# Performance work log

Hardware: AMD Instinct MI355X
Metric: run time of the kernel (lower is better)

## Reference

```python
import jax, jax.numpy as jnp
import numpy as np

D_MODEL, D_INNER, D_STATE, NHEADS, HEADDIM, D_CONV, CHUNK = 1024, 2048, 128, 32, 64, 4, 64
B_SZ, L = 2, 2048
EPS = 1e-5


def _segsum_exp(x):
    # x: (..., T) -> exp of lower-triangular cumulative segment sums, (..., T, T)
    cs = jnp.cumsum(x, axis=-1)
    seg = cs[..., :, None] - cs[..., None, :]
    T = x.shape[-1]
    mask = jnp.tril(jnp.ones((T, T), dtype=bool))
    return jnp.exp(jnp.where(mask, seg, 0.0)) * mask


def ssd(x, A, B, C, chunk):
    # x: (b,l,h,p), A: (b,l,h), B,C: (b,l,n)
    b, l, h, p = x.shape
    n = B.shape[-1]
    c = l // chunk
    x = x.reshape(b, c, chunk, h, p)
    A = A.reshape(b, c, chunk, h).transpose(0, 3, 1, 2)        # (b,h,c,s)
    B = B.reshape(b, c, chunk, n)
    C = C.reshape(b, c, chunk, n)
    A_cum = jnp.cumsum(A, axis=-1)                              # (b,h,c,s)
    Lmat = _segsum_exp(A)                                       # (b,h,c,s,s)
    # intra-chunk (diagonal block) output
    Y_diag = jnp.einsum('bcln,bcsn,bhcls,bcshp->bclhp', C, B, Lmat, x)
    # per-chunk final states
    decay_states = jnp.exp(A_cum[..., -1:] - A_cum)             # (b,h,c,s)
    states = jnp.einsum('bcsn,bhcs,bcshp->bchpn', B, decay_states, x)
    states = jnp.concatenate([jnp.zeros_like(states[:, :1]), states], axis=1)  # (b,c+1,h,p,n)
    # inter-chunk recurrence over chunk sums
    chunk_sums = jnp.pad(A_cum[..., -1], ((0, 0), (0, 0), (1, 0)))  # (b,h,c+1)
    decay_chunk = _segsum_exp(chunk_sums)                       # (b,h,c+1,c+1)
    new_states = jnp.einsum('bhzc,bchpn->bzhpn', decay_chunk, states)
    states_in, final_state = new_states[:, :-1], new_states[:, -1]
    out_decay = jnp.exp(A_cum)                                  # (b,h,c,s)
    Y_off = jnp.einsum('bcln,bchpn,bhcl->bclhp', C, states_in, out_decay)
    Y = (Y_diag + Y_off).reshape(b, l, h, p)
    return Y, final_state


def causal_depthwise_conv(x, w, b):
    # x: (B, C, L), w: (C, K), b: (C,)
    K = w.shape[-1]
    Llen = x.shape[-1]
    xp = jnp.pad(x, ((0, 0), (0, 0), (K - 1, 0)))
    out = b[None, :, None]
    for k in range(K):
        out = out + w[None, :, k, None] * xp[:, :, k:k + Llen]
    return out


def setup_inputs() -> dict:
    key = jax.random.key(0)
    ks = jax.random.split(key, 9)
    d_in_proj = 2 * D_INNER + 2 * D_STATE + NHEADS
    conv_dim = D_INNER + 2 * D_STATE
    return {
        'u': jax.random.normal(ks[0], (B_SZ, L, D_MODEL), jnp.float32),
        'W_in': jax.random.normal(ks[1], (d_in_proj, D_MODEL), jnp.float32) * (D_MODEL ** -0.5),
        'conv_w': jax.random.normal(ks[2], (conv_dim, D_CONV), jnp.float32) * (D_CONV ** -0.5),
        'conv_b': jax.random.normal(ks[3], (conv_dim,), jnp.float32) * 0.01,
        'dt_bias': jax.random.normal(ks[4], (NHEADS,), jnp.float32),
        'A_log': jnp.log(1.0 + 15.0 * jax.random.uniform(ks[5], (NHEADS,), jnp.float32)),
        'D': jax.random.normal(ks[6], (NHEADS,), jnp.float32),
        'norm_w': jnp.ones((D_INNER,), jnp.float32),
        'W_out': jax.random.normal(ks[8], (D_MODEL, D_INNER), jnp.float32) * (D_INNER ** -0.5),
    }


def reference(u, W_in, conv_w, conv_b, dt_bias, A_log, D, norm_w, W_out):
    zxbcdt = u @ W_in.T                                        # (B,L,d_in_proj)
    z = zxbcdt[..., :D_INNER]
    xBC = zxbcdt[..., D_INNER:2 * D_INNER + 2 * D_STATE]
    dt = jax.nn.softplus(zxbcdt[..., -NHEADS:] + dt_bias)      # (B,L,H)
    # causal depthwise conv + silu
    xBC = causal_depthwise_conv(xBC.transpose(0, 2, 1), conv_w, conv_b).transpose(0, 2, 1)
    xBC = jax.nn.silu(xBC)
    A = -jnp.exp(A_log)                                        # (H,)
    x = xBC[..., :D_INNER].reshape(u.shape[0], u.shape[1], NHEADS, HEADDIM)
    Bm = xBC[..., D_INNER:D_INNER + D_STATE]
    Cm = xBC[..., D_INNER + D_STATE:]
    y, _ = ssd(x * dt[..., None], A * dt, Bm, Cm, CHUNK)
    y = y + x * D[:, None]
    y = y.reshape(u.shape[0], u.shape[1], D_INNER)
    # gated RMSNorm
    y = y * jax.nn.silu(z)
    y = y * jax.lax.rsqrt(jnp.mean(y * y, axis=-1, keepdims=True) + EPS) * norm_w
    return y @ W_out.T
```

## Files before the change

### kernel.cpp

```cpp
#include <hip/hip_runtime.h>
#include <hip/hip_bf16.h>
#include <math.h>

#define D_MODEL 1024
#define D_INNER 2048
#define D_STATE 128
#define NHEADS 32
#define HEADDIM 64
#define CHUNK 64
#define B_SZ 2
#define LSEQ 2048
#define BL (B_SZ*LSEQ)
#define DPROJ (2*D_INNER + 2*D_STATE + NHEADS)
#define CONV_DIM (D_INNER + 2*D_STATE)
#define NCHUNK (LSEQ/CHUNK)
#define NPAD1 4480
#define EPSF 1e-5f

typedef __attribute__((ext_vector_type(8))) _Float16 half8;
typedef __attribute__((ext_vector_type(4))) _Float16 half4;
typedef __attribute__((ext_vector_type(4))) float f32x4;

__device__ __forceinline__ float siluf(float v){ return v / (1.0f + expf(-v)); }
__device__ __forceinline__ float softplusf(float v){ return v > 20.0f ? v : log1pf(expf(v)); }
__device__ __forceinline__ unsigned short f2h(float x){
  union { _Float16 h; unsigned short u; } v; v.h = (_Float16)x;
  return v.u;
}
__device__ __forceinline__ float h2f(unsigned short x){
  union { unsigned short u; _Float16 h; } v; v.u = x;
  return (float)v.h;
}
__device__ __forceinline__ _Float16 h2h(unsigned short x){
  union { unsigned short u; _Float16 h; } v; v.u = x;
  return v.h;
}

typedef const __attribute__((address_space(1))) void gvoid_t;
typedef __attribute__((address_space(3))) void lvoid_t;
__device__ __forceinline__ void gl_lds16(const void* gsrc, void* ldst) {
  gvoid_t* g = reinterpret_cast<gvoid_t*>((uintptr_t)gsrc);
  lvoid_t* l = reinterpret_cast<lvoid_t*>((unsigned int)(uintptr_t)ldst);
  __builtin_amdgcn_global_load_lds(g, l, 16, 0, 0);
}

__global__ void cvt_f16(const float* __restrict__ in, unsigned short* __restrict__ out, int n4) {
  int i = blockIdx.x*256 + threadIdx.x;
  if (i >= n4) return;
  float4 v = *(const float4*)(in + (size_t)i*4);
  ushort4 o; o.x=f2h(v.x); o.y=f2h(v.y); o.z=f2h(v.z); o.w=f2h(v.w);
  *(ushort4*)(out + (size_t)i*4) = o;
}

__global__ void cvt_pad(const float* __restrict__ in, unsigned short* __restrict__ out,
                        int rows_in, int total4, int kdim4) {
  int i = blockIdx.x*256 + threadIdx.x;
  if (i >= total4) return;
  int row = i / kdim4;
  ushort4 o; o.x=0; o.y=0; o.z=0; o.w=0;
  if (row < rows_in) {
    float4 v = *(const float4*)(in + (size_t)i*4);
    o.x=f2h(v.x); o.y=f2h(v.y); o.z=f2h(v.z); o.w=f2h(v.w);
  }
  *(ushort4*)(out + (size_t)i*4) = o;
}

template<int OUT_F16>
__global__ __launch_bounds__(256) void gemm_f16_pipe(const unsigned short* __restrict__ A,
    const unsigned short* __restrict__ W, void* __restrict__ Cv, int N, int K) {
  __shared__ unsigned short lds[5*2*4096];
  const int t   = threadIdx.x;
  const int wid = t >> 6, l = t & 63;
  const int nwg = gridDim.x * gridDim.y;
  int bid = blockIdx.y * gridDim.x + blockIdx.x;
  int swz = (bid & 7) * (nwg >> 3) + (bid >> 3);
  const int m0 = (swz / gridDim.x) * 128;
  const int n0 = (swz % gridDim.x) * 128;
  const int wr = wid >> 1, wc = wid & 1;
  const int fr = l & 15, cg = l >> 4;
  const int NT = K >> 5;

  int srow[2]; int scol[2];
  #pragma unroll
  for (int i=0;i<2;++i){
    int s = i*256 + t;
    int r = s >> 2, c = s & 3;
    int sw = (r + (r>>2)) & 3;
    srow[i] = r; scol[i] = (c ^ sw) * 8;
  }
  const unsigned short* Abase = A + (size_t)m0 * K;
  const unsigned short* Wbase = W + (size_t)n0 * K;

#define STAGE(tt, slot) { \
    int kk = (tt) << 5; \
    unsigned short* La = &lds[(slot)*8192]; \
    unsigned short* Lb = &lds[(slot)*8192 + 4096]; \
    gl_lds16(Abase + (size_t)srow[0]*K + kk + scol[0], (char*)La + (0*256+t)*16); \
    gl_lds16(Abase + (size_t)srow[1]*K + kk + scol[1], (char*)La + (1*256+t)*16); \
    gl_lds16(Wbase + (size_t)srow[0]*K + kk + scol[0], (char*)Lb + (0*256+t)*16); \
    gl_lds16(Wbase + (size_t)srow[1]*K + kk + scol[1], (char*)Lb + (1*256+t)*16); \
  }

  f32x4 acc[4][4] = {};
  STAGE(0, 0);
  STAGE(1, 1);
  STAGE(2, 2);
  STAGE(3, 3);
  asm volatile("s_waitcnt vmcnt(12)" ::: "memory");
  __builtin_amdgcn_s_barrier();
  asm volatile("" ::: "memory");

  int cs = 0;
  for (int tt = 0; tt < NT; ++tt) {
    int ss = (cs == 0) ? 4 : cs - 1;
    if (tt + 4 < NT) STAGE(tt+4, ss);
    const unsigned short* La = &lds[cs*8192];
    const unsigned short* Lb = &lds[cs*8192 + 4096];
    half8 af[4], bfv[4];
    #pragma unroll
    for (int m=0;m<4;++m){
      int r = wr*64 + m*16 + fr;
      int sw = (r + (r>>2)) & 3;
      af[m] = *(const half8*)&La[(r*4 + (cg ^ sw))*8];
    }
    #pragma unroll
    for (int n=0;n<4;++n){
      int r = wc*64 + n*16 + fr;
      int sw = (r + (r>>2)) & 3;
      bfv[n] = *(const half8*)&Lb[(r*4 + (cg ^ sw))*8];
    }
    __builtin_amdgcn_s_setprio(1);
    #pragma unroll
    for (int m=0;m<4;++m)
      #pragma unroll
      for (int n=0;n<4;++n)
        acc[m][n] = __builtin_amdgcn_mfma_f32_16x16x32_f16(af[m], bfv[n], acc[m][n], 0, 0, 0);
    __builtin_amdgcn_s_setprio(0);
    if (tt + 1 < NT) {
      if      (tt + 4 < NT) { asm volatile("s_waitcnt vmcnt(12)" ::: "memory"); }
      else if (tt + 3 < NT) { asm volatile("s_waitcnt vmcnt(8)"  ::: "memory"); }
      else if (tt + 2 < NT) { asm volatile("s_waitcnt vmcnt(4)"  ::: "memory"); }
      else                  { asm volatile("s_waitcnt vmcnt(0)"  ::: "memory"); }
      __builtin_amdgcn_s_barrier();
      asm volatile("" ::: "memory");
    }
    cs = (cs == 4) ? 0 : cs + 1;
  }
#undef STAGE

  const int crow = m0 + wr*64 + (l >> 4) * 4;
  const int ccol0 = n0 + wc*64 + fr;
  #pragma unroll
  for (int m = 0; m < 4; ++m) {
    #pragma unroll
    for (int n = 0; n < 4; ++n) {
      int col = ccol0 + n*16;
      if (col < N) {
        if (OUT_F16) {
          unsigned short* cp = (unsigned short*)Cv + (size_t)(crow + m*16)*N + col;
          #pragma unroll
          for (int j = 0; j < 4; ++j) cp[(size_t)j*N] = f2h(acc[m][n][j]);
        } else {
          float* cp = (float*)Cv + (size_t)(crow + m*16)*N + col;
          #pragma unroll
          for (int j = 0; j < 4; ++j) cp[(size_t)j*N] = acc[m][n][j];
        }
      }
    }
  }
}

__global__ void dtx_kernel(const unsigned short* __restrict__ zx,
    const float* __restrict__ dt_bias, float* __restrict__ dt) {
  int i = blockIdx.x*256 + threadIdx.x;
  if (i >= BL*NHEADS) return;
  int row = i >> 5, h = i & 31;
  float v = h2f(zx[(size_t)row*DPROJ + (2*D_INNER + 2*D_STATE) + h]) + dt_bias[h];
  dt[i] = softplusf(v);
}

__global__ __launch_bounds__(64) void acum_kernel(const float* __restrict__ dt,
    const float* __restrict__ A_log, float* __restrict__ A_cum) {
  int blk = blockIdx.x;
  int c = blk & 31, h = (blk >> 5) & 31, b = blk >> 10;
  int l = threadIdx.x;
  __shared__ float sv[64];
  int row = b*LSEQ + c*CHUNK + l;
  float a = -expf(A_log[h]);
  sv[l] = a * dt[row*NHEADS + h];
  __syncthreads();
  if (l == 0) {
    float s = 0.f;
    for (int i=0;i<64;++i){ s += sv[i]; sv[i] = s; }
  }
  __syncthreads();
  A_cum[blk*64 + l] = sv[l];
}

__global__ __launch_bounds__(256) void conv8_kernel(const unsigned short* __restrict__ zx,
    const float* __restrict__ w, const float* __restrict__ bias, unsigned short* __restrict__ xBC) {
  int idx = blockIdx.x*256 + threadIdx.x;
  if (idx >= (BL/8)*(CONV_DIM/4)) return;
  int c4  = idx % (CONV_DIM/4);
  int rb  = idx / (CONV_DIM/4);
  int ch  = c4 * 4;
  int row0 = rb * 8;
  int l0   = row0 & (LSEQ-1);
  float4 r[11];
  #pragma unroll
  for (int jj=0;jj<11;++jj){
    int li = l0 + jj - 3;
    if (li >= 0) {
      ushort4 v = *(const ushort4*)&zx[(size_t)(row0 + jj - 3)*DPROJ + D_INNER + ch];
      r[jj] = make_float4(h2f(v.x), h2f(v.y), h2f(v.z), h2f(v.w));
    } else r[jj] = make_float4(0.f,0.f,0.f,0.f);
  }
  float4 wv[4];
  #pragma unroll
  for (int c=0;c<4;++c) wv[c] = *(const float4*)&w[(ch+c)*4];
  float4 bv = *(const float4*)&bias[ch];
  #pragma unroll
  for (int j=0;j<8;++j){
    float4 acc = bv;
    acc.x += wv[0].x*r[j].x + wv[0].y*r[j+1].x + wv[0].z*r[j+2].x + wv[0].w*r[j+3].x;
    acc.y += wv[1].x*r[j].y + wv[1].y*r[j+1].y + wv[1].z*r[j+2].y + wv[1].w*r[j+3].y;
    acc.z += wv[2].x*r[j].z + wv[2].y*r[j+1].z + wv[2].z*r[j+2].z + wv[2].w*r[j+3].z;
    acc.w += wv[3].x*r[j].w + wv[3].y*r[j+1].w + wv[3].z*r[j+2].w + wv[3].w*r[j+3].w;
    ushort4 o; o.x=f2h(siluf(acc.x)); o.y=f2h(siluf(acc.y)); o.z=f2h(siluf(acc.z)); o.w=f2h(siluf(acc.w));
    *(ushort4*)&xBC[(size_t)(row0+j)*CONV_DIM + ch] = o;
  }
}

__global__ __launch_bounds__(256) void g_kernel(const unsigned short* __restrict__ xBC, float* __restrict__ G) {
  int blk = blockIdx.x >> 2;
  int lq  = blockIdx.x & 3;
  int b = blk >> 5, c = blk & 31;
  __shared__ float Bsh[64][129];
  int t = threadIdx.x;
  int row0 = b*LSEQ + c*CHUNK;
  for (int j=0;j<32;++j){
    int lin = j*256 + t;
    int s = lin >> 7, n = lin & 127;
    Bsh[s][n] = h2f(xBC[(size_t)(row0+s)*CONV_DIM + D_INNER + n]);
  }
  __syncthreads();
  int l = lq*16 + (t >> 4), s0 = (t & 15) * 4;
  const unsigned short* Cp = &xBC[(size_t)(row0+l)*CONV_DIM + D_INNER + D_STATE];
  float acc[4] = {};
  for (int n=0;n<128;++n){
    float cv = h2f(Cp[n]);
    #pragma unroll
    for (int j=0;j<4;++j) acc[j] += cv * Bsh[s0+j][n];
  }
  float* Gp = &G[(size_t)blk*4096 + l*64 + s0];
  #pragma unroll
  for (int j=0;j<4;++j) Gp[j] = acc[j];
}

__global__ __launch_bounds__(256) void states_mfma(const unsigned short* __restrict__ xBC,
    const float* __restrict__ dt, const float* __restrict__ A_cum, unsigned short* __restrict__ states) {
  int blk = blockIdx.x;
  int h = blk & 31, c = (blk>>5)&31, b = blk>>10;
  __shared__ _Float16 Bt[128][72];
  __shared__ _Float16 xdT[64][72];
  __shared__ float Ac[64], dtl[64];
  int t = threadIdx.x;
  int wid = t >> 6, ln = t & 63;
  int row0 = b*LSEQ + c*CHUNK;
  if (t < 64){ Ac[t] = A_cum[((b*32+h)*32 + c)*64 + t]; dtl[t] = dt[(row0+t)*NHEADS + h]; }
  __syncthreads();
  float AcL = Ac[63];
  #pragma unroll
  for (int j=0;j<32;++j){
    int lin = j*256+t; int s = lin>>7, n = lin&127;
    Bt[n][s] = h2h(xBC[(size_t)(row0+s)*CONV_DIM + D_INNER + n]);
  }
  #pragma unroll
  for (int j=0;j<16;++j){
    int lin = j*256+t; int s = lin>>6, p = lin&63;
    xdT[p][s] = (_Float16)(h2f(xBC[(size_t)(row0+s)*CONV_DIM + h*HEADDIM + p]) * dtl[s] * expf(AcL - Ac[s]));
  }
  __syncthreads();
  const int fr = ln & 15, fk = (ln >> 4) * 8;
  f32x4 acc[4][2] = {};
  #pragma unroll
  for (int ks = 0; ks < 2; ++ks){
    half8 a[4], bb[2];
    #pragma unroll
    for (int pt=0;pt<4;++pt) a[pt] = *(const half8*)&xdT[pt*16+fr][ks*32+fk];
    #pragma unroll
    for (int nt=0;nt<2;++nt) bb[nt] = *(const half8*)&Bt[(wid*2+nt)*16+fr][ks*32+fk];
    #pragma unroll
    for (int pt=0;pt<4;++pt)
      #pragma unroll
      for (int nt=0;nt<2;++nt)
        acc[pt][nt] = __builtin_amdgcn_mfma_f32_16x16x32_f16(a[pt], bb[nt], acc[pt][nt], 0, 0, 0);
  }
  unsigned short* Sp = &states[(size_t)blk*8192];
  #pragma unroll
  for (int pt=0;pt<4;++pt){
    int p0 = pt*16 + (ln>>4)*4;
    #pragma unroll
    for (int nt=0;nt<2;++nt){
      int n = (wid*2+nt)*16 + fr;
      #pragma unroll
      for (int j=0;j<4;++j) Sp[(p0+j)*128 + n] = f2h(acc[pt][nt][j]);
    }
  }
}

__global__ __launch_bounds__(256) void scan_kernel(const float* __restrict__ A_cum,
                                                   unsigned short* __restrict__ states) {
  int g  = blockIdx.x & 7;
  int bh = blockIdx.x >> 3;
  int b = bh >> 5, h = bh & 31;
  int t = threadIdx.x;
  float S[4];
  #pragma unroll
  for (int j=0;j<4;++j) S[j] = 0.f;
  for (int c=0;c<NCHUNK;++c){
    float decay = expf(A_cum[((b*32+h)*32 + c)*64 + 63]);
    unsigned short* Sp = &states[(size_t)((b*32+c)*32 + h)*8192];
    #pragma unroll
    for (int j=0;j<4;++j){
      float tmp = h2f(Sp[(g*4+j)*256+t]);
      Sp[(g*4+j)*256+t] = f2h(S[j]);
      S[j] = S[j]*decay + tmp;
    }
  }
}

__global__ __launch_bounds__(256) void y_mfma(const unsigned short* __restrict__ xBC,
    const unsigned short* __restrict__ zx, const float* __restrict__ dt,
    const float* __restrict__ A_cum, const float* __restrict__ G,
    const unsigned short* __restrict__ states, const float* __restrict__ Dp,
    unsigned short* __restrict__ y_pre) {
  int blk = blockIdx.x;
  int h = blk & 31, c = (blk>>5)&31, b = blk>>10;
  __shared__ _Float16 Cl[64][136];
  __shared__ _Float16 Sin[64][136];
  __shared__ _Float16 Ms[64][72];
  __shared__ _Float16 xdT[64][72];
  __shared__ float Ac[64], dtl[64];
  int t = threadIdx.x;
  int wid = t >> 6, ln = t & 63;
  int row0 = b*LSEQ + c*CHUNK;
  if (t < 64){ Ac[t] = A_cum[((b*32+h)*32 + c)*64 + t]; dtl[t] = dt[(row0+t)*NHEADS + h]; }
  __syncthreads();
  #pragma unroll
  for (int j=0;j<32;++j){
    int lin = j*256+t; int l = lin>>7, n = lin&127;
    Cl[l][n] = (_Float16)(h2f(xBC[(size_t)(row0+l)*CONV_DIM + D_INNER + D_STATE + n]) * expf(Ac[l]));
  }
  {
    const unsigned short* Sg = &states[(size_t)blk*8192];
    #pragma unroll
    for (int j=0;j<8;++j){
      int elem = (j*256+t)*4; int p = elem>>7, n = elem&127;
      ushort4 v = *(const ushort4*)&Sg[elem];
      half4 hv = { h2h(v.x), h2h(v.y), h2h(v.z), h2h(v.w) };
      *(half4*)&Sin[p][n] = hv;
    }
  }
  #pragma unroll
  for (int j=0;j<16;++j){
    int lin = j*256+t; int s = lin>>6, p = lin&63;
    xdT[p][s] = (_Float16)(h2f(xBC[(size_t)(row0+s)*CONV_DIM + h*HEADDIM + p]) * dtl[s]);
  }
  {
    const float* Gp = &G[(size_t)(b*32+c)*4096];
    #pragma unroll
    for (int j=0;j<16;++j){
      int lin = j*256+t; int l = lin>>6, s = lin&63;
      Ms[l][s] = (s <= l) ? (_Float16)(Gp[l*64+s] * expf(Ac[l]-Ac[s])) : (_Float16)0.f;
    }
  }
  __syncthreads();
  const int wr = wid >> 1, wc = wid & 1;
  const int fr = ln & 15, fk = (ln >> 4) * 8;
  f32x4 acc[2][2] = {};
  #pragma unroll
  for (int ks = 0; ks < 4; ++ks){
    half8 a[2], bb[2];
    #pragma unroll
    for (int lt=0;lt<2;++lt) a[lt] = *(const half8*)&Cl[(wr*2+lt)*16+fr][ks*32+fk];
    #pragma unroll
    for (int pt=0;pt<2;++pt) bb[pt] = *(const half8*)&Sin[(wc*2+pt)*16+fr][ks*32+fk];
    #pragma unroll
    for (int lt=0;lt<2;++lt)
      #pragma unroll
      for (int pt=0;pt<2;++pt)
        acc[lt][pt] = __builtin_amdgcn_mfma_f32_16x16x32_f16(a[lt], bb[pt], acc[lt][pt], 0, 0, 0);
  }
  #pragma unroll
  for (int ks = 0; ks < 2; ++ks){
    half8 a[2], bb[2];
    #pragma unroll
    for (int lt=0;lt<2;++lt) a[lt] = *(const half8*)&Ms[(wr*2+lt)*16+fr][ks*32+fk];
    #pragma unroll
    for (int pt=0;pt<2;++pt) bb[pt] = *(const half8*)&xdT[(wc*2+pt)*16+fr][ks*32+fk];
    #pragma unroll
    for (int lt=0;lt<2;++lt)
      #pragma unroll
      for (int pt=0;pt<2;++pt)
        acc[lt][pt] = __builtin_amdgcn_mfma_f32_16x16x32_f16(a[lt], bb[pt], acc[lt][pt], 0, 0, 0);
  }
  float Dh = Dp[h];
  #pragma unroll
  for (int lt=0;lt<2;++lt){
    int l0 = (wr*2+lt)*16 + (ln>>4)*4;
    #pragma unroll
    for (int pt=0;pt<2;++pt){
      int p = (wc*2+pt)*16 + fr;
      #pragma unroll
      for (int j=0;j<4;++j){
        int grow = row0 + l0 + j;
        float x = h2f(xBC[(size_t)grow*CONV_DIM + h*HEADDIM + p]);
        float z = h2f(zx[(size_t)grow*DPROJ + h*HEADDIM + p]);
        y_pre[(size_t)grow*D_INNER + h*HEADDIM + p] = f2h((acc[lt][pt][j] + x*Dh) * siluf(z));
      }
    }
  }
}

__global__ __launch_bounds__(256) void rms_kernel(const unsigned short* __restrict__ y,
    const float* __restrict__ norm_w, unsigned short* __restrict__ yh) {
  int row = blockIdx.x;
  int t = threadIdx.x;
  const unsigned short* yr = y + (size_t)row*D_INNER + t*8;
  ushort4 a = *(const ushort4*)yr;
  ushort4 bq = *(const ushort4*)(yr+4);
  float v[8];
  v[0]=h2f(a.x); v[1]=h2f(a.y); v[2]=h2f(a.z); v[3]=h2f(a.w);
  v[4]=h2f(bq.x); v[5]=h2f(bq.y); v[6]=h2f(bq.z); v[7]=h2f(bq.w);
  float ss = 0.f;
  #pragma unroll
  for (int j=0;j<8;++j) ss += v[j]*v[j];
  #pragma unroll
  for (int off=32; off>0; off>>=1) ss += __shfl_down(ss, off, 64);
  __shared__ float wsum[4];
  int wid = t >> 6, lane = t & 63;
  if (lane == 0) wsum[wid] = ss;
  __syncthreads();
  if (t == 0) wsum[0] = rsqrtf((wsum[0]+wsum[1]+wsum[2]+wsum[3])/D_INNER + EPSF);
  __syncthreads();
  float sc = wsum[0];
  float4 w0 = *(const float4*)&norm_w[t*8];
  float4 w1 = *(const float4*)&norm_w[t*8+4];
  ushort4 o0, o1;
  o0.x=f2h(v[0]*sc*w0.x); o0.y=f2h(v[1]*sc*w0.y); o0.z=f2h(v[2]*sc*w0.z); o0.w=f2h(v[3]*sc*w0.w);
  o1.x=f2h(v[4]*sc*w1.x); o1.y=f2h(v[5]*sc*w1.y); o1.z=f2h(v[6]*sc*w1.z); o1.w=f2h(v[7]*sc*w1.w);
  unsigned short* yo = yh + (size_t)row*D_INNER + t*8;
  *(ushort4*)yo = o0;
  *(ushort4*)(yo+4) = o1;
}

extern "C" void kernel_launch(void* const* d_in, const int* in_sizes, int n_in,
                              void* d_out, int out_size, void* d_ws, size_t ws_size,
                              hipStream_t stream) {
  const float* u       = (const float*)d_in[0];
  const float* W_in    = (const float*)d_in[1];
  const float* conv_w  = (const float*)d_in[2];
  const float* conv_b  = (const float*)d_in[3];
  const float* dt_bias = (const float*)d_in[4];
  const float* A_log   = (const float*)d_in[5];
  const float* Dp      = (const float*)d_in[6];
  const float* norm_w  = (const float*)d_in[7];
  const float* W_out   = (const float*)d_in[8];
  float* out = (float*)d_out;

  char* w = (char*)d_ws;
  unsigned short* zx_h   = (unsigned short*)w;  w += (size_t)BL*DPROJ*2;
  unsigned short* xBC_h  = (unsigned short*)w;  w += (size_t)BL*CONV_DIM*2;
  unsigned short* ypre_h = (unsigned short*)w;  w += (size_t)BL*D_INNER*2;
  unsigned short* y_h    = (unsigned short*)w;  w += (size_t)BL*D_INNER*2;
  unsigned short* u_h    = (unsigned short*)w;  w += (size_t)BL*D_MODEL*2;
  unsigned short* Win_h  = (unsigned short*)w;  w += (size_t)NPAD1*D_MODEL*2;
  unsigned short* Wout_h = (unsigned short*)w;  w += (size_t)D_MODEL*D_INNER*2;
  unsigned short* states = (unsigned short*)w;  w += (size_t)B_SZ*NCHUNK*NHEADS*HEADDIM*D_STATE*2;
  float* dt     = (float*)w;  w += (size_t)BL*NHEADS*4;
  float* A_cum  = (float*)w;  w += (size_t)B_SZ*NHEADS*NCHUNK*CHUNK*4;
  float* G      = (float*)w;  w += (size_t)B_SZ*NCHUNK*CHUNK*CHUNK*4;

  cvt_f16<<<(BL*D_MODEL/4)/256, 256, 0, stream>>>(u, u_h, BL*D_MODEL/4);
  cvt_pad<<<((NPAD1*D_MODEL/4)+255)/256, 256, 0, stream>>>(W_in, Win_h, DPROJ, NPAD1*D_MODEL/4, D_MODEL/4);
  cvt_f16<<<(D_MODEL*D_INNER/4)/256, 256, 0, stream>>>(W_out, Wout_h, D_MODEL*D_INNER/4);
  gemm_f16_pipe<1><<<dim3(NPAD1/128, BL/128), 256, 0, stream>>>(u_h, Win_h, zx_h, DPROJ, D_MODEL);
  dtx_kernel<<<(BL*NHEADS+255)/256, 256, 0, stream>>>(zx_h, dt_bias, dt);
  acum_kernel<<<B_SZ*NHEADS*NCHUNK, 64, 0, stream>>>(dt, A_log, A_cum);
  conv8_kernel<<<((BL/8)*(CONV_DIM/4)+255)/256, 256, 0, stream>>>(zx_h, conv_w, conv_b, xBC_h);
  g_kernel<<<B_SZ*NCHUNK*4, 256, 0, stream>>>(xBC_h, G);
  states_mfma<<<B_SZ*NCHUNK*NHEADS, 256, 0, stream>>>(xBC_h, dt, A_cum, states);
  scan_kernel<<<B_SZ*NHEADS*8, 256, 0, stream>>>(A_cum, states);
  y_mfma<<<B_SZ*NCHUNK*NHEADS, 256, 0, stream>>>(xBC_h, zx_h, dt, A_cum, G, states, Dp, ypre_h);
  rms_kernel<<<BL, 256, 0, stream>>>(ypre_h, norm_w, y_h);
  gemm_f16_pipe<0><<<dim3(D_MODEL/128, BL/128), 256, 0, stream>>>(y_h, Wout_h, out, D_MODEL, D_INNER);
}
```

Before: 210.7 us.

## Merge conversion and dt/cumsum kernels; fold RMSNorm scale into output GEMM

Three weight/input conversion kernels become one launch, and norm_w is folded into the fp16 copy of W_out. The dt softplus and A cumsum kernels merge into one kernel that uses a wave shuffle scan instead of a serial loop. The RMSNorm now computes only per-row scales and applies them in the output GEMM epilogue, which removes a full read and write of y. The GEMM pipeline also drops from 5 to 4 LDS stages, reducing shared memory per block at the cost of less prefetch depth.

```diff
diff --git a/kernel.cpp b/kernel.cpp
--- a/kernel.cpp
+++ b/kernel.cpp
@@ -44,31 +44,45 @@
   __builtin_amdgcn_global_load_lds(g, l, 16, 0, 0);
 }
 
-__global__ void cvt_f16(const float* __restrict__ in, unsigned short* __restrict__ out, int n4) {
+#define NU4  (BL*D_MODEL/4)
+#define NW4  (NPAD1*D_MODEL/4)
+#define NWo4 (D_MODEL*D_INNER/4)
+#define NCVT (NU4+NW4+NWo4)
+
+__global__ void cvt_all(const float* __restrict__ u, const float* __restrict__ W_in,
+                        const float* __restrict__ W_out, const float* __restrict__ norm_w,
+                        unsigned short* __restrict__ u_h, unsigned short* __restrict__ Win_h,
+                        unsigned short* __restrict__ Wg_h) {
   int i = blockIdx.x*256 + threadIdx.x;
-  if (i >= n4) return;
-  float4 v = *(const float4*)(in + (size_t)i*4);
-  ushort4 o; o.x=f2h(v.x); o.y=f2h(v.y); o.z=f2h(v.z); o.w=f2h(v.w);
-  *(ushort4*)(out + (size_t)i*4) = o;
-}
-
-__global__ void cvt_pad(const float* __restrict__ in, unsigned short* __restrict__ out,
-                        int rows_in, int total4, int kdim4) {
-  int i = blockIdx.x*256 + threadIdx.x;
-  if (i >= total4) return;
-  int row = i / kdim4;
-  ushort4 o; o.x=0; o.y=0; o.z=0; o.w=0;
-  if (row < rows_in) {
-    float4 v = *(const float4*)(in + (size_t)i*4);
-    o.x=f2h(v.x); o.y=f2h(v.y); o.z=f2h(v.z); o.w=f2h(v.w);
-  }
-  *(ushort4*)(out + (size_t)i*4) = o;
+  if (i >= NCVT) return;
+  if (i < NU4) {
+    float4 v = *(const float4*)(u + (size_t)i*4);
+    ushort4 o; o.x=f2h(v.x); o.y=f2h(v.y); o.z=f2h(v.z); o.w=f2h(v.w);
+    *(ushort4*)(u_h + (size_t)i*4) = o;
+  } else if (i < NU4 + NW4) {
+    int q = i - NU4;
+    int row = q / (D_MODEL/4);
+    ushort4 o; o.x=0; o.y=0; o.z=0; o.w=0;
+    if (row < DPROJ) {
+      float4 v = *(const float4*)(W_in + (size_t)q*4);
+      o.x=f2h(v.x); o.y=f2h(v.y); o.z=f2h(v.z); o.w=f2h(v.w);
+    }
+    *(ushort4*)(Win_h + (size_t)q*4) = o;
+  } else {
+    int q = i - NU4 - NW4;
+    int colq = q % (D_INNER/4);
+    float4 v = *(const float4*)(W_out + (size_t)q*4);
+    float4 g = *(const float4*)(norm_w + (size_t)colq*4);
+    ushort4 o; o.x=f2h(v.x*g.x); o.y=f2h(v.y*g.y); o.z=f2h(v.z*g.z); o.w=f2h(v.w*g.w);
+    *(ushort4*)(Wg_h + (size_t)q*4) = o;
+  }
 }
 
 template<int OUT_F16>
 __global__ __launch_bounds__(256) void gemm_f16_pipe(const unsigned short* __restrict__ A,
-    const unsigned short* __restrict__ W, void* __restrict__ Cv, int N, int K) {
-  __shared__ unsigned short lds[5*2*4096];
+    const unsigned short* __restrict__ W, void* __restrict__ Cv,
+    const float* __restrict__ Sc, int N, int K) {
+  __shared__ unsigned short lds[4*2*4096];
   const int t   = threadIdx.x;
   const int wid = t >> 6, l = t & 63;
   const int nwg = gridDim.x * gridDim.y;
@@ -105,17 +119,15 @@
   STAGE(0, 0);
   STAGE(1, 1);
   STAGE(2, 2);
-  STAGE(3, 3);
-  asm volatile("s_waitcnt vmcnt(12)" ::: "memory");
+  asm volatile("s_waitcnt vmcnt(8)" ::: "memory");
   __builtin_amdgcn_s_barrier();
   asm volatile("" ::: "memory");
 
-  int cs = 0;
   for (int tt = 0; tt < NT; ++tt) {
-    int ss = (cs == 0) ? 4 : cs - 1;
-    if (tt + 4 < NT) STAGE(tt+4, ss);
-    const unsigned short* La = &lds[cs*8192];
-    const unsigned short* Lb = &lds[cs*8192 + 4096];
+    int slot = tt & 3;
+    if (tt + 3 < NT) STAGE(tt+3, (tt+3)&3);
+    const unsigned short* La = &lds[slot*8192];
+    const unsigned short* Lb = &lds[slot*8192 + 4096];
     half8 af[4], bfv[4];
     #pragma unroll
     for (int m=0;m<4;++m){
@@ -137,14 +149,12 @@
         acc[m][n] = __builtin_amdgcn_mfma_f32_16x16x32_f16(af[m], bfv[n], acc[m][n], 0, 0, 0);
     __builtin_amdgcn_s_setprio(0);
     if (tt + 1 < NT) {
-      if      (tt + 4 < NT) { asm volatile("s_waitcnt vmcnt(12)" ::: "memory"); }
-      else if (tt + 3 < NT) { asm volatile("s_waitcnt vmcnt(8)"  ::: "memory"); }
-      else if (tt + 2 < NT) { asm volatile("s_waitcnt vmcnt(4)"  ::: "memory"); }
-      else                  { asm volatile("s_waitcnt vmcnt(0)"  ::: "memory"); }
+      if      (tt + 3 < NT) { asm volatile("s_waitcnt vmcnt(8)" ::: "memory"); }
+      else if (tt + 2 < NT) { asm volatile("s_waitcnt vmcnt(4)" ::: "memory"); }
+      else                  { asm volatile("s_waitcnt vmcnt(0)" ::: "memory"); }
       __builtin_amdgcn_s_barrier();
       asm volatile("" ::: "memory");
     }
-    cs = (cs == 4) ? 0 : cs + 1;
   }
 #undef STAGE
 
@@ -163,38 +173,30 @@
         } else {
           float* cp = (float*)Cv + (size_t)(crow + m*16)*N + col;
           #pragma unroll
-          for (int j = 0; j < 4; ++j) cp[(size_t)j*N] = acc[m][n][j];
+          for (int j = 0; j < 4; ++j) cp[(size_t)j*N] = acc[m][n][j] * Sc[crow + m*16 + j];
         }
       }
     }
   }
 }
 
-__global__ void dtx_kernel(const unsigned short* __restrict__ zx,
-    const float* __restrict__ dt_bias, float* __restrict__ dt) {
-  int i = blockIdx.x*256 + threadIdx.x;
-  if (i >= BL*NHEADS) return;
-  int row = i >> 5, h = i & 31;
-  float v = h2f(zx[(size_t)row*DPROJ + (2*D_INNER + 2*D_STATE) + h]) + dt_bias[h];
-  dt[i] = softplusf(v);
-}
-
-__global__ __launch_bounds__(64) void acum_kernel(const float* __restrict__ dt,
-    const float* __restrict__ A_log, float* __restrict__ A_cum) {
+__global__ __launch_bounds__(64) void dtacum_kernel(const unsigned short* __restrict__ zx,
+    const float* __restrict__ dt_bias, const float* __restrict__ A_log,
+    float* __restrict__ dt, float* __restrict__ A_cum) {
   int blk = blockIdx.x;
   int c = blk & 31, h = (blk >> 5) & 31, b = blk >> 10;
   int l = threadIdx.x;
-  __shared__ float sv[64];
   int row = b*LSEQ + c*CHUNK + l;
-  float a = -expf(A_log[h]);
-  sv[l] = a * dt[row*NHEADS + h];
-  __syncthreads();
-  if (l == 0) {
-    float s = 0.f;
-    for (int i=0;i<64;++i){ s += sv[i]; sv[i] = s; }
-  }
-  __syncthreads();
-  A_cum[blk*64 + l] = sv[l];
+  float v = h2f(zx[(size_t)row*DPROJ + (2*D_INNER + 2*D_STATE) + h]) + dt_bias[h];
+  float dtv = softplusf(v);
+  dt[row*NHEADS + h] = dtv;
+  float val = -expf(A_log[h]) * dtv;
+  #pragma unroll
+  for (int off = 1; off < 64; off <<= 1) {
+    float nv = __shfl_up(val, off, 64);
+    if (l >= off) val += nv;
+  }
+  A_cum[blk*64 + l] = val;
 }
 
 __global__ __launch_bounds__(256) void conv8_kernel(const unsigned short* __restrict__ zx,
@@ -423,36 +425,24 @@
   }
 }
 
-__global__ __launch_bounds__(256) void rms_kernel(const unsigned short* __restrict__ y,
-    const float* __restrict__ norm_w, unsigned short* __restrict__ yh) {
+__global__ __launch_bounds__(256) void rowsc_kernel(const unsigned short* __restrict__ y,
+                                                    float* __restrict__ sc) {
   int row = blockIdx.x;
   int t = threadIdx.x;
   const unsigned short* yr = y + (size_t)row*D_INNER + t*8;
   ushort4 a = *(const ushort4*)yr;
   ushort4 bq = *(const ushort4*)(yr+4);
-  float v[8];
-  v[0]=h2f(a.x); v[1]=h2f(a.y); v[2]=h2f(a.z); v[3]=h2f(a.w);
-  v[4]=h2f(bq.x); v[5]=h2f(bq.y); v[6]=h2f(bq.z); v[7]=h2f(bq.w);
   float ss = 0.f;
-  #pragma unroll
-  for (int j=0;j<8;++j) ss += v[j]*v[j];
+  float v;
+  v=h2f(a.x); ss+=v*v; v=h2f(a.y); ss+=v*v; v=h2f(a.z); ss+=v*v; v=h2f(a.w); ss+=v*v;
+  v=h2f(bq.x); ss+=v*v; v=h2f(bq.y); ss+=v*v; v=h2f(bq.z); ss+=v*v; v=h2f(bq.w); ss+=v*v;
   #pragma unroll
   for (int off=32; off>0; off>>=1) ss += __shfl_down(ss, off, 64);
   __shared__ float wsum[4];
   int wid = t >> 6, lane = t & 63;
   if (lane == 0) wsum[wid] = ss;
   __syncthreads();
-  if (t == 0) wsum[0] = rsqrtf((wsum[0]+wsum[1]+wsum[2]+wsum[3])/D_INNER + EPSF);
-  __syncthreads();
-  float sc = wsum[0];
-  float4 w0 = *(const float4*)&norm_w[t*8];
-  float4 w1 = *(const float4*)&norm_w[t*8+4];
-  ushort4 o0, o1;
-  o0.x=f2h(v[0]*sc*w0.x); o0.y=f2h(v[1]*sc*w0.y); o0.z=f2h(v[2]*sc*w0.z); o0.w=f2h(v[3]*sc*w0.w);
-  o1.x=f2h(v[4]*sc*w1.x); o1.y=f2h(v[5]*sc*w1.y); o1.z=f2h(v[6]*sc*w1.z); o1.w=f2h(v[7]*sc*w1.w);
-  unsigned short* yo = yh + (size_t)row*D_INNER + t*8;
-  *(ushort4*)yo = o0;
-  *(ushort4*)(yo+4) = o1;
+  if (t == 0) sc[row] = rsqrtf((wsum[0]+wsum[1]+wsum[2]+wsum[3])/D_INNER + EPSF);
 }
 
 extern "C" void kernel_launch(void* const* d_in, const int* in_sizes, int n_in,
@@ -473,26 +463,23 @@
   unsigned short* zx_h   = (unsigned short*)w;  w += (size_t)BL*DPROJ*2;
   unsigned short* xBC_h  = (unsigned short*)w;  w += (size_t)BL*CONV_DIM*2;
   unsigned short* ypre_h = (unsigned short*)w;  w += (size_t)BL*D_INNER*2;
-  unsigned short* y_h    = (unsigned short*)w;  w += (size_t)BL*D_INNER*2;
   unsigned short* u_h    = (unsigned short*)w;  w += (size_t)BL*D_MODEL*2;
   unsigned short* Win_h  = (unsigned short*)w;  w += (size_t)NPAD1*D_MODEL*2;
-  unsigned short* Wout_h = (unsigned short*)w;  w += (size_t)D_MODEL*D_INNER*2;
+  unsigned short* Wg_h   = (unsigned short*)w;  w += (size_t)D_MODEL*D_INNER*2;
   unsigned short* states = (unsigned short*)w;  w += (size_t)B_SZ*NCHUNK*NHEADS*HEADDIM*D_STATE*2;
   float* dt     = (float*)w;  w += (size_t)BL*NHEADS*4;
   float* A_cum  = (float*)w;  w += (size_t)B_SZ*NHEADS*NCHUNK*CHUNK*4;
   float* G      = (float*)w;  w += (size_t)B_SZ*NCHUNK*CHUNK*CHUNK*4;
-
-  cvt_f16<<<(BL*D_MODEL/4)/256, 256, 0, stream>>>(u, u_h, BL*D_MODEL/4);
-  cvt_pad<<<((NPAD1*D_MODEL/4)+255)/256, 256, 0, stream>>>(W_in, Win_h, DPROJ, NPAD1*D_MODEL/4, D_MODEL/4);
-  cvt_f16<<<(D_MODEL*D_INNER/4)/256, 256, 0, stream>>>(W_out, Wout_h, D_MODEL*D_INNER/4);
-  gemm_f16_pipe<1><<<dim3(NPAD1/128, BL/128), 256, 0, stream>>>(u_h, Win_h, zx_h, DPROJ, D_MODEL);
-  dtx_kernel<<<(BL*NHEADS+255)/256, 256, 0, stream>>>(zx_h, dt_bias, dt);
-  acum_kernel<<<B_SZ*NHEADS*NCHUNK, 64, 0, stream>>>(dt, A_log, A_cum);
+  float* sc     = (float*)w;  w += (size_t)BL*4;
+
+  cvt_all<<<(NCVT+255)/256, 256, 0, stream>>>(u, W_in, W_out, norm_w, u_h, Win_h, Wg_h);
+  gemm_f16_pipe<1><<<dim3(NPAD1/128, BL/128), 256, 0, stream>>>(u_h, Win_h, zx_h, nullptr, DPROJ, D_MODEL);
+  dtacum_kernel<<<B_SZ*NHEADS*NCHUNK, 64, 0, stream>>>(zx_h, dt_bias, A_log, dt, A_cum);
   conv8_kernel<<<((BL/8)*(CONV_DIM/4)+255)/256, 256, 0, stream>>>(zx_h, conv_w, conv_b, xBC_h);
   g_kernel<<<B_SZ*NCHUNK*4, 256, 0, stream>>>(xBC_h, G);
   states_mfma<<<B_SZ*NCHUNK*NHEADS, 256, 0, stream>>>(xBC_h, dt, A_cum, states);
   scan_kernel<<<B_SZ*NHEADS*8, 256, 0, stream>>>(A_cum, states);
   y_mfma<<<B_SZ*NCHUNK*NHEADS, 256, 0, stream>>>(xBC_h, zx_h, dt, A_cum, G, states, Dp, ypre_h);
-  rms_kernel<<<BL, 256, 0, stream>>>(ypre_h, norm_w, y_h);
-  gemm_f16_pipe<0><<<dim3(D_MODEL/128, BL/128), 256, 0, stream>>>(y_h, Wout_h, out, D_MODEL, D_INNER);
-}
+  rowsc_kernel<<<BL, 256, 0, stream>>>(ypre_h, sc);
+  gemm_f16_pipe<0><<<dim3(D_MODEL/128, BL/128), 256, 0, stream>>>(ypre_h, Wg_h, out, sc, D_MODEL, D_INNER);
+}
```

Result: no change. 208.0 us (-1.3%).
